# Optimization experiments

Measured on AMD Instinct MI355X. Metric: run time of the kernel, lower is better.

Reference implementation:

```python
import jax, jax.numpy as jnp
import numpy as np

IN_CH, OUT_CH, KS = 64, 128, 3
GRID, DEG = 8, 3
STRIDE, PAD = 1, 1
SIZE = IN_CH * KS * KS            # 576
NCOEF = GRID + DEG                # 11
GRID_RANGE = (-1.0, 1.0)


def _xavier_uniform(key, shape):
    fan_out, fan_in = shape
    a = float(np.sqrt(6.0 / (fan_in + fan_out)))
    return jax.random.uniform(key, shape, minval=-a, maxval=a, dtype=jnp.float32)


def setup_inputs() -> dict:
    key = jax.random.key(0)
    k1, k2, k3 = jax.random.split(key, 3)
    x = jax.random.normal(k1, (8, IN_CH, 32, 32), dtype=jnp.float32)
    # non-trainable knot grid, one row per unfolded feature
    knots = jnp.tile(jnp.linspace(GRID_RANGE[0], GRID_RANGE[1], GRID + 1, dtype=jnp.float32)[None, :], (SIZE, 1))
    coeff = 0.1 * jax.random.normal(k2, (OUT_CH, SIZE, NCOEF), dtype=jnp.float32)
    base_weights = _xavier_uniform(k3, (OUT_CH, SIZE))
    spline_weights = jnp.ones((OUT_CH, SIZE), dtype=jnp.float32)
    return {"x": x, "knots": knots, "coeff": coeff,
            "base_weights": base_weights, "spline_weights": spline_weights}


def bspline_basis(x, grid, k):
    # x: (S, P) evaluation points; grid: (S, G+1) knots. Returns (S, G+k, P).
    h = (grid[:, -1:] - grid[:, :1]) / (grid.shape[1] - 1)
    left = grid[:, :1] - h * jnp.arange(k, 0, -1, dtype=x.dtype)
    right = grid[:, -1:] + h * jnp.arange(1, k + 1, dtype=x.dtype)
    g = jnp.concatenate([left, grid, right], axis=1)  # (S, G+1+2k)
    xe = x[:, None, :]
    B = ((xe >= g[:, :-1, None]) & (xe < g[:, 1:, None])).astype(x.dtype)
    for d in range(1, k + 1):  # de Boor recursion over fixed degree
        B = ((xe - g[:, :-(d + 1), None]) / (g[:, d:-1, None] - g[:, :-(d + 1), None]) * B[:, :-1]
             + (g[:, d + 1:, None] - xe) / (g[:, d + 1:, None] - g[:, 1:-d, None]) * B[:, 1:])
    return B


def _unfold(x):
    # torch F.unfold with channel-major (c, kh, kw) feature ordering
    N, C, H, W = x.shape
    xp = jnp.pad(x, ((0, 0), (0, 0), (PAD, PAD), (PAD, PAD)))
    Hp = (H + 2 * PAD - KS) // STRIDE + 1
    Wp = (W + 2 * PAD - KS) // STRIDE + 1
    patches = jnp.stack([xp[:, :, i:i + STRIDE * Hp:STRIDE, j:j + STRIDE * Wp:STRIDE]
                         for i in range(KS) for j in range(KS)], axis=2)  # (N, C, KS*KS, Hp, Wp)
    L = Hp * Wp
    u = patches.reshape(N, SIZE, L)              # (N, size, L)
    u = jnp.transpose(u, (1, 0, 2)).reshape(SIZE, N * L)  # (size, N*L), col = n*L + l
    return u, Hp, Wp


def reference(x, knots, coeff, base_weights, spline_weights):
    N = x.shape[0]
    u, Hp, Wp = _unfold(x)                                   # (size, P)
    base = base_weights @ jax.nn.silu(u)                     # (Cout, P)
    B = bspline_basis(u, knots, DEG)                         # (size, ncoef, P)
    eff = spline_weights[:, :, None] * coeff                 # (Cout, size, ncoef)
    spl = jnp.einsum('csj,sjp->cp', eff, B)                  # (Cout, P)
    out = (base + spl).reshape(OUT_CH, N, Hp, Wp)
    return jnp.transpose(out, (1, 0, 2, 3))                  # (N, Cout, Hp, Wp)
```

## Files before the change

kernel.cpp:

```cpp
#include <hip/hip_runtime.h>


typedef __attribute__((ext_vector_type(8))) short bf16x8;
typedef __attribute__((ext_vector_type(4))) float f32x4;

#define ACT_PLANE 591872
#define WSWZ_BYTES 1769472
#define ACT_BYTES  14204928
#define PART_OFF   (WSWZ_BYTES + ACT_BYTES)

__device__ __forceinline__ short f2bf(float f) {
    union { float f; unsigned u; } c; c.f = f;
    unsigned r = c.u + 0x7fffu + ((c.u >> 16) & 1u);
    return (short)(r >> 16);
}

__global__ void kan_weights(const float* __restrict__ coeff,
                            const float* __restrict__ basew,
                            const float* __restrict__ splw,
                            short* __restrict__ Wswz) {
    __shared__ float coeffL[6336];
    __shared__ float basewL[576];
    __shared__ float splwL[576];
    const int co = blockIdx.x;
    const int t  = threadIdx.x;
    const float* crow = coeff + co * 6336;
    for (int i = t; i < 6336; i += 256) coeffL[i] = crow[i];
    for (int i = t; i < 576; i += 256) {
        basewL[i] = basew[co * 576 + i];
        splwL[i]  = splw[co * 576 + i];
    }
    __syncthreads();
    const int cb = co >> 4, lm = co & 15;
    for (int c = t; c < 864; c += 256) {
        int kk = c >> 2, quad = c & 3;
        int f  = kk / 18;
        int rm = kk - f * 18;
        int tap = rm >> 1, ks = rm & 1;
        bf16x8 pack;
#pragma unroll
        for (int j = 0; j < 8; ++j) {
            int ci = ks * 32 + quad * 8 + j;
            int s  = ci * 9 + tap;
            float v = (f == 0) ? basewL[s] : splwL[s] * coeffL[s * 11 + (f - 1)];
            pack[j] = f2bf(v);
        }
        *(bf16x8*)(Wswz + ((kk * 8 + cb) * 64 + quad * 16 + lm) * 8) = pack;
    }
}

__global__ void kan_act(const float* __restrict__ x,
                        short* __restrict__ act) {
    __shared__ float xrow[64][33];
    const int b  = blockIdx.x;
    const int n  = b / 34;
    const int yp = b - n * 34;
    const int t  = threadIdx.x;
    const int y  = yp - 1;

    if (y >= 0 && y < 32) {
        for (int i = t; i < 2048; i += 256) {
            int ci = i >> 5, xx = i & 31;
            xrow[ci][xx] = x[((n * 64 + ci) * 32 + y) * 32 + xx];
        }
    }
    __syncthreads();

    for (int g = t; g < 272; g += 256) {
        int xp = g >> 3, c0 = (g & 7) * 8;
        bool interior = (y >= 0 && y < 32 && xp >= 1 && xp <= 32);
        bf16x8 packs[12];
#pragma unroll
        for (int j = 0; j < 8; ++j) {
            float v = interior ? xrow[c0 + j][xp - 1] : 0.f;
            float sig  = 1.f / (1.f + expf(-v));
            float silu = v * sig;
            float tt = 4.f * v + 7.f;
            int   i0 = -100;
            float b0 = 0.f, b1 = 0.f, b2 = 0.f, b3 = 0.f;
            if (tt >= 0.f && tt < 14.f) {
                i0 = (int)tt;
                float fr  = tt - (float)i0;
                float omf = 1.f - fr;
                float fr2 = fr * fr, fr3 = fr2 * fr;
                b0 = omf * omf * omf * (1.f / 6.f);
                b1 = (3.f * fr3 - 6.f * fr2 + 4.f) * (1.f / 6.f);
                b2 = (-3.f * fr3 + 3.f * fr2 + 3.f * fr + 1.f) * (1.f / 6.f);
                b3 = fr3 * (1.f / 6.f);
            }
            packs[0][j] = f2bf(silu);
#pragma unroll
            for (int f = 1; f <= 11; ++f) {
                int jj = f - 1;
                float val = 0.f;
                val = (jj == i0 - 3) ? b0 : val;
                val = (jj == i0 - 2) ? b1 : val;
                val = (jj == i0 - 1) ? b2 : val;
                val = (jj == i0    ) ? b3 : val;
                packs[f][j] = f2bf(val);
            }
        }
        long base = ((long)((n * 1156) + yp * 34 + xp)) * 64 + c0;
#pragma unroll
        for (int f = 0; f < 12; ++f)
            *(bf16x8*)(act + (long)f * ACT_PLANE + base) = packs[f];
    }
}

__global__ __launch_bounds__(256, 2)
void kan_gemm(const short* __restrict__ Wswz,
              const short* __restrict__ act,
              float* __restrict__ part) {
    __shared__ short ldsB[2][13056];

    const int t    = threadIdx.x;
    const int w    = t >> 6;
    const int l    = t & 63;
    const int lp   = l & 15;
    const int quad = l >> 4;

    const int bz    = blockIdx.x;
    const int fg    = bz & 3;
    const int cb2   = (bz >> 2) & 1;
    const int ptile = bz >> 3;
    const int n     = ptile >> 3;
    const int y0    = (ptile & 7) << 2;

    {
        const int f0 = fg * 3;
        const uint4* slab = (const uint4*)(act + (((f0 * 8 + n) * 1156) + y0 * 34) * 64);
        uint4* ldsv = (uint4*)ldsB[0];
#pragma unroll
        for (int it = 0; it < 7; ++it) {
            int cg = t + it * 256;
            if (cg < 1632) {
                int pix = cg >> 3, sub = cg & 7;
                ldsv[pix * 8 + (sub ^ (pix & 7))] = slab[cg];
            }
        }
    }
    __syncthreads();

    f32x4 acc[4][2];
#pragma unroll
    for (int m = 0; m < 4; ++m)
#pragma unroll
        for (int nt = 0; nt < 2; ++nt) {
            f32x4 z = {0.f, 0.f, 0.f, 0.f};
            acc[m][nt] = z;
        }

#pragma unroll 1
    for (int p = 0; p < 3; ++p) {
        const int f = fg * 3 + p;

        if (p < 2) {
            const uint4* slab = (const uint4*)(act + ((((f + 1) * 8 + n) * 1156) + y0 * 34) * 64);
            uint4* ldsv = (uint4*)ldsB[(p + 1) & 1];
#pragma unroll
            for (int it = 0; it < 7; ++it) {
                int cg = t + it * 256;
                if (cg < 1632) {
                    int pix = cg >> 3, sub = cg & 7;
                    ldsv[pix * 8 + (sub ^ (pix & 7))] = slab[cg];
                }
            }
        }

        const short* B0 = ldsB[p & 1];
        const short* Af = Wswz + (long)(f * 18) * 4096;

#pragma unroll
        for (int kk = 0; kk < 18; ++kk) {
            const int tap = kk >> 1, ks = kk & 1;
            const int dy  = tap / 3;
            const int dx  = tap - dy * 3;
            const short* Ak = Af + kk * 4096 + (cb2 * 4) * 512 + l * 8;
            bf16x8 a0 = *(const bf16x8*)(Ak);
            bf16x8 a1 = *(const bf16x8*)(Ak + 512);
            bf16x8 a2 = *(const bf16x8*)(Ak + 1024);
            bf16x8 a3 = *(const bf16x8*)(Ak + 1536);
            const int c = ks * 4 + quad;
#pragma unroll
            for (int nt = 0; nt < 2; ++nt) {
                int pix = (w + dy) * 34 + (nt << 4) + lp + dx;
                bf16x8 b = *(const bf16x8*)&B0[pix * 64 + ((c ^ (pix & 7)) << 3)];
                acc[0][nt] = __builtin_amdgcn_mfma_f32_16x16x32_bf16(a0, b, acc[0][nt], 0, 0, 0);
                acc[1][nt] = __builtin_amdgcn_mfma_f32_16x16x32_bf16(a1, b, acc[1][nt], 0, 0, 0);
                acc[2][nt] = __builtin_amdgcn_mfma_f32_16x16x32_bf16(a2, b, acc[2][nt], 0, 0, 0);
                acc[3][nt] = __builtin_amdgcn_mfma_f32_16x16x32_bf16(a3, b, acc[3][nt], 0, 0, 0);
            }
        }
        __syncthreads();
    }

    float* dst = part + (long)fg * 1048576;
#pragma unroll
    for (int m = 0; m < 4; ++m)
#pragma unroll
        for (int nt = 0; nt < 2; ++nt)
#pragma unroll
            for (int r = 0; r < 4; ++r) {
                int co = cb2 * 64 + m * 16 + quad * 4 + r;
                int y  = y0 + w;
                int xx = (nt << 4) + lp;
                dst[((long)(n * 128 + co) * 32 + y) * 32 + xx] = acc[m][nt][r];
            }
}

__global__ void kan_reduce(const float* __restrict__ part,
                           float* __restrict__ out) {
    int g = blockIdx.x * 256 + threadIdx.x;
    f32x4 a = ((const f32x4*)part)[g];
#pragma unroll
    for (int s = 1; s < 4; ++s)
        a += ((const f32x4*)(part + (long)s * 1048576))[g];
    ((f32x4*)out)[g] = a;
}

extern "C" void kernel_launch(void* const* d_in, const int* in_sizes, int n_in,
                              void* d_out, int out_size, void* d_ws, size_t ws_size,
                              hipStream_t stream) {
    const float* x     = (const float*)d_in[0];
    const float* coeff = (const float*)d_in[2];
    const float* basew = (const float*)d_in[3];
    const float* splw  = (const float*)d_in[4];
    float* out = (float*)d_out;

    short* Wswz = (short*)d_ws;
    short* act  = (short*)((char*)d_ws + WSWZ_BYTES);
    float* part = (float*)((char*)d_ws + PART_OFF);

    kan_weights<<<128, 256, 0, stream>>>(coeff, basew, splw, Wswz);
    kan_act<<<272, 256, 0, stream>>>(x, act);
    kan_gemm<<<512, 256, 0, stream>>>(Wswz, act, part);
    kan_reduce<<<1024, 256, 0, stream>>>(part, out);
}
```

Baseline: 119.4 us.

## Fuse B-spline activation computation into GEMM kernel, dropping act buffer

Removes the separate kan_act kernel and its large bf16 activation tensor (12 feature planes). Each GEMM block now loads its own input rows of x (with halo), converts them to bf16 in LDS, and computes only its 3 feature planes (SiLU or B-spline basis) straight into shared memory. The block tile also changes from 4 rows × 64 output channels to 2 rows × all 128 channels, split across warps. This saves global write and read traffic and one launch, at the cost of recomputing halo rows, using more LDS, and rounding x to bf16 before the basis is evaluated, which can shift interval indices slightly.

New measurement: 108.6 us. -9.1%, faster.

```diff
diff --git a/kernel.cpp b/kernel.cpp
--- a/kernel.cpp
+++ b/kernel.cpp
@@ -3,16 +3,19 @@
 
 typedef __attribute__((ext_vector_type(8))) short bf16x8;
 typedef __attribute__((ext_vector_type(4))) float f32x4;
-
-#define ACT_PLANE 591872
+typedef __attribute__((ext_vector_type(4))) unsigned short u16x4;
+
 #define WSWZ_BYTES 1769472
-#define ACT_BYTES  14204928
-#define PART_OFF   (WSWZ_BYTES + ACT_BYTES)
+#define PART_OFF   WSWZ_BYTES
 
 __device__ __forceinline__ short f2bf(float f) {
     union { float f; unsigned u; } c; c.f = f;
     unsigned r = c.u + 0x7fffu + ((c.u >> 16) & 1u);
     return (short)(r >> 16);
+}
+__device__ __forceinline__ float bf2f(unsigned short u) {
+    union { unsigned u; float f; } c; c.u = ((unsigned)u) << 16;
+    return c.f;
 }
 
 __global__ void kan_weights(const float* __restrict__ coeff,
@@ -49,30 +52,54 @@
     }
 }
 
-__global__ void kan_act(const float* __restrict__ x,
-                        short* __restrict__ act) {
-    __shared__ float xrow[64][33];
-    const int b  = blockIdx.x;
-    const int n  = b / 34;
-    const int yp = b - n * 34;
-    const int t  = threadIdx.x;
-    const int y  = yp - 1;
-
-    if (y >= 0 && y < 32) {
-        for (int i = t; i < 2048; i += 256) {
-            int ci = i >> 5, xx = i & 31;
-            xrow[ci][xx] = x[((n * 64 + ci) * 32 + y) * 32 + xx];
-        }
+__global__ __launch_bounds__(256, 2)
+void kan_gemm(const float* __restrict__ x,
+              const short* __restrict__ Wswz,
+              float* __restrict__ part) {
+    __shared__ unsigned short xs[4 * 64 * 36];
+    __shared__ short Bs[3 * 8704];
+
+    const int t    = threadIdx.x;
+    const int w    = t >> 6;
+    const int l    = t & 63;
+    const int lp   = l & 15;
+    const int quad = l >> 4;
+    const int wm   = w >> 1;
+    const int wn   = w & 1;
+
+    const int bz    = blockIdx.x;
+    const int fg    = bz & 3;
+    const int ptile = bz >> 2;
+    const int n     = ptile >> 4;
+    const int y0    = (ptile & 15) << 1;
+
+#pragma unroll
+    for (int it = 0; it < 8; ++it) {
+        int cg = t + it * 256;
+        int rr = cg >> 9, ci = (cg >> 3) & 63, q = cg & 7;
+        int y  = y0 - 1 + rr;
+        f32x4 v = {0.f, 0.f, 0.f, 0.f};
+        if (y >= 0 && y < 32)
+            v = *(const f32x4*)(x + (((n * 64 + ci) * 32 + y) * 32 + q * 4));
+        u16x4 p;
+        p.x = (unsigned short)f2bf(v.x); p.y = (unsigned short)f2bf(v.y);
+        p.z = (unsigned short)f2bf(v.z); p.w = (unsigned short)f2bf(v.w);
+        *(u16x4*)&xs[(rr * 64 + ci) * 36 + q * 4] = p;
     }
     __syncthreads();
 
-    for (int g = t; g < 272; g += 256) {
-        int xp = g >> 3, c0 = (g & 7) * 8;
-        bool interior = (y >= 0 && y < 32 && xp >= 1 && xp <= 32);
-        bf16x8 packs[12];
+    const int f0 = fg * 3;
+    for (int it = t; it < 1088; it += 256) {
+        int rr  = it >> 8;
+        int rem = it - rr * 272;
+        rr  = it / 272;
+        rem = it - rr * 272;
+        int xp = rem >> 3, cch = rem & 7, c0 = cch << 3;
+        bool interior = (xp >= 1 && xp <= 32);
+        bf16x8 packs[3];
 #pragma unroll
         for (int j = 0; j < 8; ++j) {
-            float v = interior ? xrow[c0 + j][xp - 1] : 0.f;
+            float v = interior ? bf2f(xs[(rr * 64 + c0 + j) * 36 + (xp - 1)]) : 0.f;
             float sig  = 1.f / (1.f + expf(-v));
             float silu = v * sig;
             float tt = 4.f * v + 7.f;
@@ -88,56 +115,27 @@
                 b2 = (-3.f * fr3 + 3.f * fr2 + 3.f * fr + 1.f) * (1.f / 6.f);
                 b3 = fr3 * (1.f / 6.f);
             }
-            packs[0][j] = f2bf(silu);
-#pragma unroll
-            for (int f = 1; f <= 11; ++f) {
-                int jj = f - 1;
-                float val = 0.f;
-                val = (jj == i0 - 3) ? b0 : val;
-                val = (jj == i0 - 2) ? b1 : val;
-                val = (jj == i0 - 1) ? b2 : val;
-                val = (jj == i0    ) ? b3 : val;
-                packs[f][j] = f2bf(val);
-            }
-        }
-        long base = ((long)((n * 1156) + yp * 34 + xp)) * 64 + c0;
-#pragma unroll
-        for (int f = 0; f < 12; ++f)
-            *(bf16x8*)(act + (long)f * ACT_PLANE + base) = packs[f];
-    }
-}
-
-__global__ __launch_bounds__(256, 2)
-void kan_gemm(const short* __restrict__ Wswz,
-              const short* __restrict__ act,
-              float* __restrict__ part) {
-    __shared__ short ldsB[2][13056];
-
-    const int t    = threadIdx.x;
-    const int w    = t >> 6;
-    const int l    = t & 63;
-    const int lp   = l & 15;
-    const int quad = l >> 4;
-
-    const int bz    = blockIdx.x;
-    const int fg    = bz & 3;
-    const int cb2   = (bz >> 2) & 1;
-    const int ptile = bz >> 3;
-    const int n     = ptile >> 3;
-    const int y0    = (ptile & 7) << 2;
-
-    {
-        const int f0 = fg * 3;
-        const uint4* slab = (const uint4*)(act + (((f0 * 8 + n) * 1156) + y0 * 34) * 64);
-        uint4* ldsv = (uint4*)ldsB[0];
-#pragma unroll
-        for (int it = 0; it < 7; ++it) {
-            int cg = t + it * 256;
-            if (cg < 1632) {
-                int pix = cg >> 3, sub = cg & 7;
-                ldsv[pix * 8 + (sub ^ (pix & 7))] = slab[cg];
-            }
-        }
+#pragma unroll
+            for (int p = 0; p < 3; ++p) {
+                int f = f0 + p;
+                float val;
+                if (f == 0) val = silu;
+                else {
+                    int jj = f - 1;
+                    val = 0.f;
+                    val = (jj == i0 - 3) ? b0 : val;
+                    val = (jj == i0 - 2) ? b1 : val;
+                    val = (jj == i0 - 1) ? b2 : val;
+                    val = (jj == i0    ) ? b3 : val;
+                }
+                packs[p][j] = f2bf(val);
+            }
+        }
+        int pix = rr * 34 + xp;
+        int swz = (cch ^ (pix & 7)) << 3;
+#pragma unroll
+        for (int p = 0; p < 3; ++p)
+            *(bf16x8*)&Bs[p * 8704 + pix * 64 + swz] = packs[p];
     }
     __syncthreads();
 
@@ -152,30 +150,14 @@
 
 #pragma unroll 1
     for (int p = 0; p < 3; ++p) {
-        const int f = fg * 3 + p;
-
-        if (p < 2) {
-            const uint4* slab = (const uint4*)(act + ((((f + 1) * 8 + n) * 1156) + y0 * 34) * 64);
-            uint4* ldsv = (uint4*)ldsB[(p + 1) & 1];
-#pragma unroll
-            for (int it = 0; it < 7; ++it) {
-                int cg = t + it * 256;
-                if (cg < 1632) {
-                    int pix = cg >> 3, sub = cg & 7;
-                    ldsv[pix * 8 + (sub ^ (pix & 7))] = slab[cg];
-                }
-            }
-        }
-
-        const short* B0 = ldsB[p & 1];
-        const short* Af = Wswz + (long)(f * 18) * 4096;
-
+        const short* B0 = Bs + p * 8704;
+        const short* Af = Wswz + (long)((f0 + p) * 18) * 4096;
 #pragma unroll
         for (int kk = 0; kk < 18; ++kk) {
             const int tap = kk >> 1, ks = kk & 1;
             const int dy  = tap / 3;
             const int dx  = tap - dy * 3;
-            const short* Ak = Af + kk * 4096 + (cb2 * 4) * 512 + l * 8;
+            const short* Ak = Af + kk * 4096 + (wm * 4) * 512 + l * 8;
             bf16x8 a0 = *(const bf16x8*)(Ak);
             bf16x8 a1 = *(const bf16x8*)(Ak + 512);
             bf16x8 a2 = *(const bf16x8*)(Ak + 1024);
@@ -183,7 +165,7 @@
             const int c = ks * 4 + quad;
 #pragma unroll
             for (int nt = 0; nt < 2; ++nt) {
-                int pix = (w + dy) * 34 + (nt << 4) + lp + dx;
+                int pix = (wn + dy) * 34 + (nt << 4) + lp + dx;
                 bf16x8 b = *(const bf16x8*)&B0[pix * 64 + ((c ^ (pix & 7)) << 3)];
                 acc[0][nt] = __builtin_amdgcn_mfma_f32_16x16x32_bf16(a0, b, acc[0][nt], 0, 0, 0);
                 acc[1][nt] = __builtin_amdgcn_mfma_f32_16x16x32_bf16(a1, b, acc[1][nt], 0, 0, 0);
@@ -191,7 +173,6 @@
                 acc[3][nt] = __builtin_amdgcn_mfma_f32_16x16x32_bf16(a3, b, acc[3][nt], 0, 0, 0);
             }
         }
-        __syncthreads();
     }
 
     float* dst = part + (long)fg * 1048576;
@@ -201,8 +182,8 @@
         for (int nt = 0; nt < 2; ++nt)
 #pragma unroll
             for (int r = 0; r < 4; ++r) {
-                int co = cb2 * 64 + m * 16 + quad * 4 + r;
-                int y  = y0 + w;
+                int co = wm * 64 + m * 16 + quad * 4 + r;
+                int y  = y0 + wn;
                 int xx = (nt << 4) + lp;
                 dst[((long)(n * 128 + co) * 32 + y) * 32 + xx] = acc[m][nt][r];
             }
@@ -228,11 +209,9 @@
     float* out = (float*)d_out;
 
     short* Wswz = (short*)d_ws;
-    short* act  = (short*)((char*)d_ws + WSWZ_BYTES);
     float* part = (float*)((char*)d_ws + PART_OFF);
 
     kan_weights<<<128, 256, 0, stream>>>(coeff, basew, splw, Wswz);
-    kan_act<<<272, 256, 0, stream>>>(x, act);
-    kan_gemm<<<512, 256, 0, stream>>>(Wswz, act, part);
+    kan_gemm<<<512, 256, 0, stream>>>(x, Wswz, part);
     kan_reduce<<<1024, 256, 0, stream>>>(part, out);
 }
```
